# Kernel tuning notes

Measured on AMD Instinct MI355X. Metric: run time of the kernel, lower is better.

Reference implementation:

```python
import jax, jax.numpy as jnp
import numpy as np

H = 16  # num_heads

def setup_inputs() -> dict:
    key = jax.random.key(0)
    ks = jax.random.split(key, 6)
    B, T, C, S = 2, 2048, 1024, 2048
    return {
        "q": jax.random.normal(ks[0], (B, T, C), jnp.float32),
        "k_xl": jax.random.normal(ks[1], (B, S, C), jnp.float32),
        "v_xl": jax.random.normal(ks[2], (B, S, C), jnp.float32),
        "W_qkv": jax.random.normal(ks[3], (3 * C, C), jnp.float32) * (1.0 / np.sqrt(C)),
        "W_proj": jax.random.normal(ks[4], (C, C), jnp.float32) * (1.0 / np.sqrt(C)),
        "pos_emb": jax.random.normal(ks[5], (S, C), jnp.float32),
        "is_causal": 0,
    }

def reference(q, k_xl, v_xl, W_qkv, W_proj, pos_emb, is_causal):
    B, T, C = q.shape
    hd = C // H
    # self_attention: W_qkv(q).split(d_model, -1)
    qkv = jnp.einsum('btc,dc->btd', q, W_qkv)  # [B,T,3C]
    qn, kn, vn = jnp.split(qkv, 3, axis=-1)
    # XL cache gets positional embedding added before use
    kx = k_xl + pos_emb[None, :, :]            # [B,S,C]
    vx = v_xl

    def to_heads(x):
        b, s, c = x.shape
        return x.reshape(b, s, H, hd).transpose(0, 2, 1, 3)  # [B,H,s,hd]

    qh = to_heads(qn)
    kcat = jnp.concatenate([to_heads(kx), to_heads(kn)], axis=2)  # [B,H,S+T,hd]
    vcat = jnp.concatenate([to_heads(vx), to_heads(vn)], axis=2)
    scale = 1.0 / jnp.sqrt(jnp.asarray(hd, qh.dtype))
    scores = jnp.einsum('bhtd,bhsd->bhts', qh, kcat) * scale  # [B,H,T,S+T]
    attn = jax.nn.softmax(scores, axis=-1)
    y = jnp.einsum('bhts,bhsd->bhtd', attn, vcat)  # [B,H,T,hd]
    y = y.transpose(0, 2, 1, 3).reshape(B, T, C)
    return jnp.einsum('btc,dc->btd', y, W_proj)
```

## Files before the change

kernel.cpp:

```cpp
#include <hip/hip_runtime.h>

typedef unsigned short u16;
typedef unsigned int u32;
typedef u16 u16x4 __attribute__((ext_vector_type(4)));
typedef u16 u16x8 __attribute__((ext_vector_type(8)));
typedef __bf16 bf16x8 __attribute__((ext_vector_type(8)));
typedef float f32x4 __attribute__((ext_vector_type(4)));
typedef float f32x16 __attribute__((ext_vector_type(16)));

static __device__ __forceinline__ u16 f2bf(float f) {
  union { float f; u32 u; } x; x.f = f;
  u32 r = x.u + 0x7fffu + ((x.u >> 16) & 1u);
  return (u16)(r >> 16);
}
static __device__ __forceinline__ u32 packbf(float a, float b) {
  union { u32 u; __bf16 h[2]; } x; x.h[0] = (__bf16)a; x.h[1] = (__bf16)b; return x.u;
}
static __device__ __forceinline__ void pl32swap(u32& a, u32& b) {
  asm volatile("v_permlane32_swap_b32 %0, %1" : "+v"(a), "+v"(b));
}
static __device__ __forceinline__ void gload16(const void* g, void* l) {
  __builtin_amdgcn_global_load_lds((const __attribute__((address_space(1))) unsigned int*)g,
                                   (__attribute__((address_space(3))) unsigned int*)l, 16, 0, 0);
}

__global__ __launch_bounds__(256) void cvt_fuse(const float* __restrict__ q, const float* __restrict__ wqkv_f,
                                                const float* __restrict__ wproj_f, const float* __restrict__ k_xl,
                                                const float* __restrict__ pos, u16* __restrict__ qbf,
                                                u16* __restrict__ wqkv, u16* __restrict__ wproj,
                                                u16* __restrict__ khxl, float sc) {
  int i = blockIdx.x * 256 + threadIdx.x;
  if (i < 2097152) {
    const float* src;
    u16* dst;
    int j;
    float s = 1.0f;
    if (i < 1048576) { src = q; dst = qbf; j = i; }
    else if (i < 1835008) { j = i - 1048576; src = wqkv_f; dst = wqkv; if (j < 262144) s = sc; }
    else { j = i - 1835008; src = wproj_f; dst = wproj; }
    float4 v = reinterpret_cast<const float4*>(src)[j];
    u16x4 o; o[0] = f2bf(v.x * s); o[1] = f2bf(v.y * s); o[2] = f2bf(v.z * s); o[3] = f2bf(v.w * s);
    reinterpret_cast<u16x4*>(dst)[j] = o;
  } else {
    int idx = i - 2097152;
    int d8 = idx & 7;
    int s = (idx >> 3) & 2047;
    int bh = idx >> 14;
    int b = bh >> 4, h = bh & 15;
    size_t src = ((size_t)(b * 2048 + s)) * 1024 + h * 64 + d8 * 8;
    size_t ps = ((size_t)s) * 1024 + h * 64 + d8 * 8;
    float4 a0 = *(const float4*)&k_xl[src];
    float4 a1 = *(const float4*)&k_xl[src + 4];
    float4 p0 = *(const float4*)&pos[ps];
    float4 p1 = *(const float4*)&pos[ps + 4];
    u16x8 o;
    o[0] = f2bf(a0.x + p0.x); o[1] = f2bf(a0.y + p0.y); o[2] = f2bf(a0.z + p0.z); o[3] = f2bf(a0.w + p0.w);
    o[4] = f2bf(a1.x + p1.x); o[5] = f2bf(a1.y + p1.y); o[6] = f2bf(a1.z + p1.z); o[7] = f2bf(a1.w + p1.w);
    *(u16x8*)&khxl[((size_t)bh * 2048 + s) * 64 + d8 * 8] = o;
  }
}

template <int OUT_BF16>
__global__ __launch_bounds__(256, 2) void gemm_bt4(const u16* __restrict__ A, const u16* __restrict__ B,
                                                   void* __restrict__ Cout, int M, int N, int K) {
  __shared__ alignas(128) u16 As[2][8192];
  __shared__ alignas(128) u16 Bs[2][8192];
  const int tid = threadIdx.x;
  const int nbx = gridDim.x;
  const int nwg = nbx * gridDim.y;
  const int id = blockIdx.x + blockIdx.y * nbx;
  const int swz = (id & 7) * (nwg >> 3) + (id >> 3);
  const int m0 = (swz / nbx) * 128, n0 = (swz % nbx) * 128;
  const int wid = tid >> 6, lane = tid & 63;
  const int lm = lane & 15, lg = lane >> 4;
  const int wm = (wid >> 1) * 64, wn = (wid & 1) * 64;
  int srow[4], scol[4], dsto[4];
#pragma unroll
  for (int i = 0; i < 4; i++) {
    int li = tid + i * 256;
    srow[i] = li >> 3;
    scol[i] = ((li & 7) ^ (srow[i] & 7)) * 8;
    dsto[i] = (i * 256 + wid * 64) * 8;
  }
  f32x4 acc[4][4] = {};
#pragma unroll
  for (int i = 0; i < 4; i++) {
    gload16(&A[(size_t)(m0 + srow[i]) * K + scol[i]], &As[0][dsto[i]]);
    gload16(&B[(size_t)(n0 + srow[i]) * K + scol[i]], &Bs[0][dsto[i]]);
  }
  int cur = 0;
  for (int k0 = 0; k0 < K; k0 += 64) {
    __syncthreads();
    if (k0 + 64 < K) {
#pragma unroll
      for (int i = 0; i < 4; i++) {
        gload16(&A[(size_t)(m0 + srow[i]) * K + k0 + 64 + scol[i]], &As[cur ^ 1][dsto[i]]);
        gload16(&B[(size_t)(n0 + srow[i]) * K + k0 + 64 + scol[i]], &Bs[cur ^ 1][dsto[i]]);
      }
    }
    const u16* Asb = As[cur];
    const u16* Bsb = Bs[cur];
#pragma unroll
    for (int ks = 0; ks < 2; ks++) {
      bf16x8 af[4], bfr[4];
#pragma unroll
      for (int mi = 0; mi < 4; mi++) {
        int row = wm + mi * 16 + lm;
        af[mi] = *(const bf16x8*)&Asb[row * 64 + (((ks * 4 + lg) ^ (row & 7)) << 3)];
      }
#pragma unroll
      for (int ni = 0; ni < 4; ni++) {
        int row = wn + ni * 16 + lm;
        bfr[ni] = *(const bf16x8*)&Bsb[row * 64 + (((ks * 4 + lg) ^ (row & 7)) << 3)];
      }
#pragma unroll
      for (int mi = 0; mi < 4; mi++)
#pragma unroll
        for (int ni = 0; ni < 4; ni++)
          acc[mi][ni] = __builtin_amdgcn_mfma_f32_16x16x32_bf16(af[mi], bfr[ni], acc[mi][ni], 0, 0, 0);
    }
    cur ^= 1;
  }
#pragma unroll
  for (int mi = 0; mi < 4; mi++)
#pragma unroll
    for (int ni = 0; ni < 4; ni++)
#pragma unroll
      for (int r = 0; r < 4; r++) {
        int row = m0 + wm + mi * 16 + lg * 4 + r;
        int col = n0 + wn + ni * 16 + lm;
        if (OUT_BF16) ((u16*)Cout)[(size_t)row * N + col] = f2bf(acc[mi][ni][r]);
        else          ((float*)Cout)[(size_t)row * N + col] = acc[mi][ni][r];
      }
}

__global__ __launch_bounds__(256) void build_vt(const float* __restrict__ v_xl, const u16* __restrict__ qkvb,
                                                u16* __restrict__ Vt) {
  __shared__ u16 tile[64][72];
  const int bh = blockIdx.y, b = bh >> 4, h = bh & 15;
  const int s0 = blockIdx.x * 64;
  const int tid = threadIdx.x;
  {
    int sl = tid >> 2;
    int dseg = (tid & 3) * 16;
    if (s0 < 2048) {
      const float* src = v_xl + ((size_t)(b * 2048 + s0 + sl)) * 1024 + h * 64 + dseg;
#pragma unroll
      for (int j = 0; j < 16; j += 4) {
        float4 v = *(const float4*)&src[j];
        tile[sl][dseg + j] = f2bf(v.x);
        tile[sl][dseg + j + 1] = f2bf(v.y);
        tile[sl][dseg + j + 2] = f2bf(v.z);
        tile[sl][dseg + j + 3] = f2bf(v.w);
      }
    } else {
      const u16* src = qkvb + ((size_t)(b * 2048 + s0 - 2048 + sl)) * 3072 + 2048 + h * 64 + dseg;
      *(u16x8*)&tile[sl][dseg] = *(const u16x8*)&src[0];
      *(u16x8*)&tile[sl][dseg + 8] = *(const u16x8*)&src[8];
    }
  }
  __syncthreads();
  {
    int d = tid >> 2;
    int sseg = (tid & 3) * 16;
    u16* dst = Vt + ((size_t)bh * 64 + d) * 4096 + s0 + sseg;
    u16x8 o0, o1;
#pragma unroll
    for (int j = 0; j < 8; j++) { o0[j] = tile[sseg + j][d]; o1[j] = tile[sseg + 8 + j][d]; }
    *(u16x8*)&dst[0] = o0;
    *(u16x8*)&dst[8] = o1;
  }
}

__global__ __launch_bounds__(256, 2) void attn_fwd10(const u16* __restrict__ qkvb, const u16* __restrict__ khxl,
                                                     const u16* __restrict__ vt, u16* __restrict__ Y) {
  const int T = 2048;
  __shared__ alignas(128) u16 lds[16384];
  __shared__ float CBl[128];
  const int dd = blockIdx.x + (blockIdx.y << 4);
  const int w = ((dd & 7) << 6) + (dd >> 3);
  const int bh = w >> 4;
  const int q0 = (w & 15) * 128;
  const int tid = threadIdx.x, wid = tid >> 6, lane = tid & 63;
  const int qt = wid >> 1, ks = wid & 1;
  const int l31 = lane & 31, hi = lane >> 5;
  const int sw = l31 & 7;
  const int b = bh >> 4, h = bh & 15;
  bf16x8 qf0[4], qf1[4];
  {
    const u16* Qp0 = qkvb + (size_t)(b * T + q0 + qt * 64 + l31) * 3072 + h * 64;
    const u16* Qp1 = Qp0 + (size_t)32 * 3072;
#pragma unroll
    for (int c = 0; c < 4; c++) {
      qf0[c] = *(const bf16x8*)&Qp0[c * 16 + hi * 8];
      qf1[c] = *(const bf16x8*)&Qp1[c * 16 + hi * 8];
    }
  }
  const int srow = tid >> 3, pc = tid & 7;
  const int scol = (pc ^ (srow & 7)) * 8;
  const u16* kxl_s = khxl + ((size_t)bh * 2048 + srow) * 64 + scol;
  const u16* knew_s = qkvb + (size_t)(b * T + srow) * 3072 + 1024 + h * 64 + scol;
  const u16* v_s = vt + ((size_t)bh * 64 + srow) * 4096 + scol;
  const int kd = tid * 8;
  f32x16 acc00 = {0.0f}, acc01 = {0.0f}, acc10 = {0.0f}, acc11 = {0.0f};
  float lrun0 = 0.0f, lrun1 = 0.0f;
  const int krow = ks * 32 + l31;

#define STAGE_XL(KO, VO)                              \
  do {                                                \
    gload16(kxl_s, &lds[(KO) + kd]);                  \
    gload16(kxl_s + 2048, &lds[(KO) + 2048 + kd]);    \
    gload16(v_s, &lds[(VO) + kd]);                    \
    gload16(v_s + 131072, &lds[(VO) + 2048 + kd]);    \
    kxl_s += 4096; v_s += 64;                         \
  } while (0)
#define STAGE_NEW(KO, VO)                             \
  do {                                                \
    gload16(knew_s, &lds[(KO) + kd]);                 \
    gload16(knew_s + 98304, &lds[(KO) + 2048 + kd]);  \
    gload16(v_s, &lds[(VO) + kd]);                    \
    gload16(v_s + 131072, &lds[(VO) + 2048 + kd]);    \
    knew_s += 196608; v_s += 64;                      \
  } while (0)
#define COMPUTE(KO, VO)                                                             \
  do {                                                                              \
    bf16x8 kf0 = *(const bf16x8*)&lds[(KO) + krow * 64 + (((0 + hi) ^ sw) << 3)];   \
    bf16x8 kf1 = *(const bf16x8*)&lds[(KO) + krow * 64 + (((2 + hi) ^ sw) << 3)];   \
    bf16x8 kf2 = *(const bf16x8*)&lds[(KO) + krow * 64 + (((4 + hi) ^ sw) << 3)];   \
    bf16x8 kf3 = *(const bf16x8*)&lds[(KO) + krow * 64 + (((6 + hi) ^ sw) << 3)];   \
    f32x16 s0 = {0.0f}, s1 = {0.0f};                                                \
    __builtin_amdgcn_s_setprio(1);                                                  \
    s0 = __builtin_amdgcn_mfma_f32_32x32x16_bf16(kf0, qf0[0], s0, 0, 0, 0);         \
    s1 = __builtin_amdgcn_mfma_f32_32x32x16_bf16(kf0, qf1[0], s1, 0, 0, 0);         \
    s0 = __builtin_amdgcn_mfma_f32_32x32x16_bf16(kf1, qf0[1], s0, 0, 0, 0);         \
    s1 = __builtin_amdgcn_mfma_f32_32x32x16_bf16(kf1, qf1[1], s1, 0, 0, 0);         \
    s0 = __builtin_amdgcn_mfma_f32_32x32x16_bf16(kf2, qf0[2], s0, 0, 0, 0);         \
    s1 = __builtin_amdgcn_mfma_f32_32x32x16_bf16(kf2, qf1[2], s1, 0, 0, 0);         \
    s0 = __builtin_amdgcn_mfma_f32_32x32x16_bf16(kf3, qf0[3], s0, 0, 0, 0);         \
    s1 = __builtin_amdgcn_mfma_f32_32x32x16_bf16(kf3, qf1[3], s1, 0, 0, 0);         \
    __builtin_amdgcn_s_setprio(0);                                                  \
    u32 w40[4][2], w41[4][2];                                                       \
    _Pragma("unroll")                                                               \
    for (int r = 0; r < 16; r++) s0[r] = __builtin_amdgcn_exp2f(s0[r]);             \
    lrun0 += (((s0[0] + s0[1]) + (s0[2] + s0[3])) + ((s0[4] + s0[5]) + (s0[6] + s0[7])))         \
           + (((s0[8] + s0[9]) + (s0[10] + s0[11])) + ((s0[12] + s0[13]) + (s0[14] + s0[15])));  \
    _Pragma("unroll")                                                               \
    for (int g = 0; g < 4; g++) {                                                   \
      w40[g][0] = packbf(s0[4 * g + 0], s0[4 * g + 1]);                             \
      w40[g][1] = packbf(s0[4 * g + 2], s0[4 * g + 3]);                             \
    }                                                                               \
    _Pragma("unroll")                                                               \
    for (int r = 0; r < 16; r++) s1[r] = __builtin_amdgcn_exp2f(s1[r]);             \
    lrun1 += (((s1[0] + s1[1]) + (s1[2] + s1[3])) + ((s1[4] + s1[5]) + (s1[6] + s1[7])))         \
           + (((s1[8] + s1[9]) + (s1[10] + s1[11])) + ((s1[12] + s1[13]) + (s1[14] + s1[15])));  \
    _Pragma("unroll")                                                               \
    for (int g = 0; g < 4; g++) {                                                   \
      w41[g][0] = packbf(s1[4 * g + 0], s1[4 * g + 1]);                             \
      w41[g][1] = packbf(s1[4 * g + 2], s1[4 * g + 3]);                             \
    }                                                                               \
    __builtin_amdgcn_s_setprio(1);                                                  \
    _Pragma("unroll")                                                               \
    for (int m2 = 0; m2 < 2; m2++) {                                                \
      int cg = 2 * (ks * 2 + m2) + hi;                                              \
      bf16x8 v0 = *(const bf16x8*)&lds[(VO) + l31 * 64 + ((cg ^ sw) << 3)];         \
      bf16x8 v1 = *(const bf16x8*)&lds[(VO) + (32 + l31) * 64 + ((cg ^ sw) << 3)];  \
      u32 A0 = w40[2 * m2][0], A2 = w40[2 * m2 + 1][0];                             \
      pl32swap(A0, A2);                                                             \
      u32 A1 = w40[2 * m2][1], A3 = w40[2 * m2 + 1][1];                             \
      pl32swap(A1, A3);                                                             \
      union { u32 u[4]; bf16x8 v; } pf0;                                            \
      pf0.u[0] = A0; pf0.u[1] = A1; pf0.u[2] = A2; pf0.u[3] = A3;                   \
      acc00 = __builtin_amdgcn_mfma_f32_32x32x16_bf16(v0, pf0.v, acc00, 0, 0, 0);   \
      acc01 = __builtin_amdgcn_mfma_f32_32x32x16_bf16(v1, pf0.v, acc01, 0, 0, 0);   \
      u32 B0 = w41[2 * m2][0], B2 = w41[2 * m2 + 1][0];                             \
      pl32swap(B0, B2);                                                             \
      u32 B1 = w41[2 * m2][1], B3 = w41[2 * m2 + 1][1];                             \
      pl32swap(B1, B3);                                                             \
      union { u32 u[4]; bf16x8 v; } pf1;                                            \
      pf1.u[0] = B0; pf1.u[1] = B1; pf1.u[2] = B2; pf1.u[3] = B3;                   \
      acc10 = __builtin_amdgcn_mfma_f32_32x32x16_bf16(v0, pf1.v, acc10, 0, 0, 0);   \
      acc11 = __builtin_amdgcn_mfma_f32_32x32x16_bf16(v1, pf1.v, acc11, 0, 0, 0);   \
    }                                                                               \
    __builtin_amdgcn_s_setprio(0);                                                  \
  } while (0)

  STAGE_XL(0, 8192);
  for (int j = 0; j < 15; ++j) {
    __syncthreads();
    STAGE_XL(4096, 12288);
    COMPUTE(0, 8192);
    __syncthreads();
    STAGE_XL(0, 8192);
    COMPUTE(4096, 12288);
  }
  __syncthreads();
  STAGE_XL(4096, 12288);
  COMPUTE(0, 8192);
  __syncthreads();
  STAGE_NEW(0, 8192);
  COMPUTE(4096, 12288);
  for (int j = 0; j < 15; ++j) {
    __syncthreads();
    STAGE_NEW(4096, 12288);
    COMPUTE(0, 8192);
    __syncthreads();
    STAGE_NEW(0, 8192);
    COMPUTE(4096, 12288);
  }
  __syncthreads();
  STAGE_NEW(4096, 12288);
  COMPUTE(0, 8192);
  __syncthreads();
  COMPUTE(4096, 12288);
#undef STAGE_XL
#undef STAGE_NEW
#undef COMPUTE

  float lt0 = lrun0 + __shfl_xor(lrun0, 32);
  float lt1 = lrun1 + __shfl_xor(lrun1, 32);
  __syncthreads();
  float* CB = (float*)lds;
  if (ks) {
    float* p0 = CB + (size_t)(qt * 2 + 0) * 64 * 32 + (size_t)lane * 32;
    float* p1 = CB + (size_t)(qt * 2 + 1) * 64 * 32 + (size_t)lane * 32;
#pragma unroll
    for (int j = 0; j < 8; j++) {
      f32x4 u0, u1;
#pragma unroll
      for (int e = 0; e < 4; e++) {
        u0[e] = (j < 4) ? acc00[4 * j + e] : acc01[4 * (j - 4) + e];
        u1[e] = (j < 4) ? acc10[4 * j + e] : acc11[4 * (j - 4) + e];
      }
      *(f32x4*)&p0[4 * (j ^ (lane & 7))] = u0;
      *(f32x4*)&p1[4 * (j ^ (lane & 7))] = u1;
    }
    if (hi == 0) {
      CBl[(qt * 2 + 0) * 32 + l31] = lt0;
      CBl[(qt * 2 + 1) * 32 + l31] = lt1;
    }
  }
  __syncthreads();
  if (!ks) {
    const float* p0 = CB + (size_t)(qt * 2 + 0) * 64 * 32 + (size_t)lane * 32;
    const float* p1 = CB + (size_t)(qt * 2 + 1) * 64 * 32 + (size_t)lane * 32;
#pragma unroll
    for (int j = 0; j < 8; j++) {
      f32x4 u0 = *(const f32x4*)&p0[4 * (j ^ (lane & 7))];
      f32x4 u1 = *(const f32x4*)&p1[4 * (j ^ (lane & 7))];
#pragma unroll
      for (int e = 0; e < 4; e++) {
        if (j < 4) { acc00[4 * j + e] += u0[e]; acc10[4 * j + e] += u1[e]; }
        else       { acc01[4 * (j - 4) + e] += u0[e]; acc11[4 * (j - 4) + e] += u1[e]; }
      }
    }
    lt0 += CBl[(qt * 2 + 0) * 32 + l31];
    lt1 += CBl[(qt * 2 + 1) * 32 + l31];
    float inv0 = 1.0f / lt0;
    float inv1 = 1.0f / lt1;
#pragma unroll
    for (int qb = 0; qb < 2; qb++) {
      float inv = qb ? inv1 : inv0;
      u16* Ts = (u16*)((char*)lds + (qt * 2 + qb) * 8192);
#pragma unroll
      for (int dt = 0; dt < 2; dt++)
#pragma unroll
        for (int r2 = 0; r2 < 4; r2++) {
          u16x4 o;
#pragma unroll
          for (int e = 0; e < 4; e++) {
            float v;
            if (qb == 0) v = dt ? acc01[4 * r2 + e] : acc00[4 * r2 + e];
            else         v = dt ? acc11[4 * r2 + e] : acc10[4 * r2 + e];
            o[e] = f2bf(v * inv);
          }
          int dbase = dt * 32 + r2 * 8 + hi * 4;
          int byteoff = l31 * 128 + ((dbase * 2) ^ (sw << 4));
          *(u16x4*)((char*)Ts + byteoff) = o;
        }
#pragma unroll
      for (int p4 = 0; p4 < 4; p4++) {
        int row = p4 * 8 + (lane >> 3);
        int c16 = lane & 7;
        u16x8 v = *(const u16x8*)((const char*)Ts + row * 128 + ((c16 << 4) ^ ((row & 7) << 4)));
        *(u16x8*)&Y[((size_t)(b * T + q0 + qt * 64 + qb * 32 + row)) * 1024 + h * 64 + c16 * 8] = v;
      }
    }
  }
}

extern "C" void kernel_launch(void* const* d_in, const int* in_sizes, int n_in,
                              void* d_out, int out_size, void* d_ws, size_t ws_size,
                              hipStream_t stream) {
  const float* q = (const float*)d_in[0];
  const float* k_xl = (const float*)d_in[1];
  const float* v_xl = (const float*)d_in[2];
  const float* W_qkv = (const float*)d_in[3];
  const float* W_proj = (const float*)d_in[4];
  const float* pos = (const float*)d_in[5];

  u16* wqkv = (u16*)d_ws;
  u16* wproj = wqkv + (size_t)3072 * 1024;
  u16* qbf = wproj + (size_t)1024 * 1024;
  u16* qkvb = qbf + (size_t)4096 * 1024;
  u16* khxl = qkvb + (size_t)4096 * 3072;
  u16* vt = khxl + (size_t)4 * 1024 * 1024;
  u16* ybf = vt + (size_t)8 * 1024 * 1024;

  const float SC = 0.125f * 1.4426950408889634f;

  cvt_fuse<<<10240, 256, 0, stream>>>(q, W_qkv, W_proj, k_xl, pos, qbf, wqkv, wproj, khxl, SC);

  gemm_bt4<1><<<dim3(24, 32), 256, 0, stream>>>(qbf, wqkv, qkvb, 4096, 3072, 1024);

  build_vt<<<dim3(64, 32), 256, 0, stream>>>(v_xl, qkvb, vt);

  attn_fwd10<<<dim3(16, 32), 256, 0, stream>>>(qkvb, khxl, vt, ybf);

  gemm_bt4<0><<<dim3(8, 32), 256, 0, stream>>>(ybf, wproj, d_out, 4096, 1024, 1024);
}
```

Before: 164.2 us.

## Split attention over XL and new key halves with separate combine kernel

Adds an attention kernel that gives each query tile two blocks, one for the XL-cache half of the keys and one for the new-token half. Each block writes unnormalised fp32 partial outputs and row sums to workspace, and a small combine kernel adds the two halves, normalises and writes bf16. The aim is more parallelism and shorter per-block serial loops. The cost is an extra launch plus fp32 partial traffic to and from global memory. This path runs only when the workspace is large enough; otherwise the original fused kernel is used.

```diff
diff --git a/kernel.cpp b/kernel.cpp
--- a/kernel.cpp
+++ b/kernel.cpp
@@ -172,57 +172,7 @@
   }
 }
 
-__global__ __launch_bounds__(256, 2) void attn_fwd10(const u16* __restrict__ qkvb, const u16* __restrict__ khxl,
-                                                     const u16* __restrict__ vt, u16* __restrict__ Y) {
-  const int T = 2048;
-  __shared__ alignas(128) u16 lds[16384];
-  __shared__ float CBl[128];
-  const int dd = blockIdx.x + (blockIdx.y << 4);
-  const int w = ((dd & 7) << 6) + (dd >> 3);
-  const int bh = w >> 4;
-  const int q0 = (w & 15) * 128;
-  const int tid = threadIdx.x, wid = tid >> 6, lane = tid & 63;
-  const int qt = wid >> 1, ks = wid & 1;
-  const int l31 = lane & 31, hi = lane >> 5;
-  const int sw = l31 & 7;
-  const int b = bh >> 4, h = bh & 15;
-  bf16x8 qf0[4], qf1[4];
-  {
-    const u16* Qp0 = qkvb + (size_t)(b * T + q0 + qt * 64 + l31) * 3072 + h * 64;
-    const u16* Qp1 = Qp0 + (size_t)32 * 3072;
-#pragma unroll
-    for (int c = 0; c < 4; c++) {
-      qf0[c] = *(const bf16x8*)&Qp0[c * 16 + hi * 8];
-      qf1[c] = *(const bf16x8*)&Qp1[c * 16 + hi * 8];
-    }
-  }
-  const int srow = tid >> 3, pc = tid & 7;
-  const int scol = (pc ^ (srow & 7)) * 8;
-  const u16* kxl_s = khxl + ((size_t)bh * 2048 + srow) * 64 + scol;
-  const u16* knew_s = qkvb + (size_t)(b * T + srow) * 3072 + 1024 + h * 64 + scol;
-  const u16* v_s = vt + ((size_t)bh * 64 + srow) * 4096 + scol;
-  const int kd = tid * 8;
-  f32x16 acc00 = {0.0f}, acc01 = {0.0f}, acc10 = {0.0f}, acc11 = {0.0f};
-  float lrun0 = 0.0f, lrun1 = 0.0f;
-  const int krow = ks * 32 + l31;
-
-#define STAGE_XL(KO, VO)                              \
-  do {                                                \
-    gload16(kxl_s, &lds[(KO) + kd]);                  \
-    gload16(kxl_s + 2048, &lds[(KO) + 2048 + kd]);    \
-    gload16(v_s, &lds[(VO) + kd]);                    \
-    gload16(v_s + 131072, &lds[(VO) + 2048 + kd]);    \
-    kxl_s += 4096; v_s += 64;                         \
-  } while (0)
-#define STAGE_NEW(KO, VO)                             \
-  do {                                                \
-    gload16(knew_s, &lds[(KO) + kd]);                 \
-    gload16(knew_s + 98304, &lds[(KO) + 2048 + kd]);  \
-    gload16(v_s, &lds[(VO) + kd]);                    \
-    gload16(v_s + 131072, &lds[(VO) + 2048 + kd]);    \
-    knew_s += 196608; v_s += 64;                      \
-  } while (0)
-#define COMPUTE(KO, VO)                                                             \
+#define ATTN_COMPUTE(KO, VO)                                                        \
   do {                                                                              \
     bf16x8 kf0 = *(const bf16x8*)&lds[(KO) + krow * 64 + (((0 + hi) ^ sw) << 3)];   \
     bf16x8 kf1 = *(const bf16x8*)&lds[(KO) + krow * 64 + (((2 + hi) ^ sw) << 3)];   \
@@ -284,37 +234,224 @@
     __builtin_amdgcn_s_setprio(0);                                                  \
   } while (0)
 
+__global__ __launch_bounds__(256, 2) void attn_split(const u16* __restrict__ qkvb, const u16* __restrict__ khxl,
+                                                     const u16* __restrict__ vt, float* __restrict__ gpart,
+                                                     float* __restrict__ gl) {
+  const int T = 2048;
+  __shared__ alignas(128) u16 lds[16384];
+  __shared__ float CBl[128];
+  const int z = blockIdx.z;
+  const int dd = blockIdx.x + (blockIdx.y << 4);
+  const int w = ((dd & 7) << 6) + (dd >> 3);
+  const int bh = w >> 4;
+  const int q0 = (w & 15) * 128;
+  const int tid = threadIdx.x, wid = tid >> 6, lane = tid & 63;
+  const int qt = wid >> 1, ks = wid & 1;
+  const int l31 = lane & 31, hi = lane >> 5;
+  const int sw = l31 & 7;
+  const int b = bh >> 4, h = bh & 15;
+  bf16x8 qf0[4], qf1[4];
+  {
+    const u16* Qp0 = qkvb + (size_t)(b * T + q0 + qt * 64 + l31) * 3072 + h * 64;
+    const u16* Qp1 = Qp0 + (size_t)32 * 3072;
+#pragma unroll
+    for (int c = 0; c < 4; c++) {
+      qf0[c] = *(const bf16x8*)&Qp0[c * 16 + hi * 8];
+      qf1[c] = *(const bf16x8*)&Qp1[c * 16 + hi * 8];
+    }
+  }
+  const int srow = tid >> 3, pc = tid & 7;
+  const int scol = (pc ^ (srow & 7)) * 8;
+  const u16* kp = z ? (qkvb + (size_t)(b * T + srow) * 3072 + 1024 + h * 64 + scol)
+                    : (khxl + ((size_t)bh * 2048 + srow) * 64 + scol);
+  const size_t kstep = z ? (size_t)196608 : (size_t)4096;
+  const size_t kc2  = z ? (size_t)98304 : (size_t)2048;
+  const u16* v_s = vt + ((size_t)bh * 64 + srow) * 4096 + z * 2048 + scol;
+  const int kd = tid * 8;
+  f32x16 acc00 = {0.0f}, acc01 = {0.0f}, acc10 = {0.0f}, acc11 = {0.0f};
+  float lrun0 = 0.0f, lrun1 = 0.0f;
+  const int krow = ks * 32 + l31;
+
+#define STAGE_Z(KO, VO)                               \
+  do {                                                \
+    gload16(kp, &lds[(KO) + kd]);                     \
+    gload16(kp + kc2, &lds[(KO) + 2048 + kd]);        \
+    gload16(v_s, &lds[(VO) + kd]);                    \
+    gload16(v_s + 131072, &lds[(VO) + 2048 + kd]);    \
+    kp += kstep; v_s += 64;                           \
+  } while (0)
+
+  STAGE_Z(0, 8192);
+  for (int j = 0; j < 15; ++j) {
+    __syncthreads();
+    STAGE_Z(4096, 12288);
+    ATTN_COMPUTE(0, 8192);
+    __syncthreads();
+    STAGE_Z(0, 8192);
+    ATTN_COMPUTE(4096, 12288);
+  }
+  __syncthreads();
+  STAGE_Z(4096, 12288);
+  ATTN_COMPUTE(0, 8192);
+  __syncthreads();
+  ATTN_COMPUTE(4096, 12288);
+#undef STAGE_Z
+
+  float lt0 = lrun0 + __shfl_xor(lrun0, 32);
+  float lt1 = lrun1 + __shfl_xor(lrun1, 32);
+  __syncthreads();
+  float* CB = (float*)lds;
+  if (ks) {
+    float* p0 = CB + (size_t)(qt * 2 + 0) * 64 * 32 + (size_t)lane * 32;
+    float* p1 = CB + (size_t)(qt * 2 + 1) * 64 * 32 + (size_t)lane * 32;
+#pragma unroll
+    for (int j = 0; j < 8; j++) {
+      f32x4 u0, u1;
+#pragma unroll
+      for (int e = 0; e < 4; e++) {
+        u0[e] = (j < 4) ? acc00[4 * j + e] : acc01[4 * (j - 4) + e];
+        u1[e] = (j < 4) ? acc10[4 * j + e] : acc11[4 * (j - 4) + e];
+      }
+      *(f32x4*)&p0[4 * (j ^ (lane & 7))] = u0;
+      *(f32x4*)&p1[4 * (j ^ (lane & 7))] = u1;
+    }
+    if (hi == 0) {
+      CBl[(qt * 2 + 0) * 32 + l31] = lt0;
+      CBl[(qt * 2 + 1) * 32 + l31] = lt1;
+    }
+  }
+  __syncthreads();
+  if (!ks) {
+    const float* p0 = CB + (size_t)(qt * 2 + 0) * 64 * 32 + (size_t)lane * 32;
+    const float* p1 = CB + (size_t)(qt * 2 + 1) * 64 * 32 + (size_t)lane * 32;
+#pragma unroll
+    for (int j = 0; j < 8; j++) {
+      f32x4 u0 = *(const f32x4*)&p0[4 * (j ^ (lane & 7))];
+      f32x4 u1 = *(const f32x4*)&p1[4 * (j ^ (lane & 7))];
+#pragma unroll
+      for (int e = 0; e < 4; e++) {
+        if (j < 4) { acc00[4 * j + e] += u0[e]; acc10[4 * j + e] += u1[e]; }
+        else       { acc01[4 * (j - 4) + e] += u0[e]; acc11[4 * (j - 4) + e] += u1[e]; }
+      }
+    }
+    lt0 += CBl[(qt * 2 + 0) * 32 + l31];
+    lt1 += CBl[(qt * 2 + 1) * 32 + l31];
+    float* gp = gpart + (size_t)z * (32u * 2048 * 64) + ((size_t)bh * 2048 + q0 + qt * 64) * 64;
+#pragma unroll
+    for (int r = 0; r < 16; r++) {
+      int d = (r & 3) + 8 * (r >> 2) + 4 * hi;
+      gp[(size_t)l31 * 64 + d]             = acc00[r];
+      gp[(size_t)l31 * 64 + 32 + d]        = acc01[r];
+      gp[(size_t)(32 + l31) * 64 + d]      = acc10[r];
+      gp[(size_t)(32 + l31) * 64 + 32 + d] = acc11[r];
+    }
+    if (hi == 0) {
+      float* glp = gl + (size_t)z * (32u * 2048) + (size_t)bh * 2048 + q0 + qt * 64;
+      glp[l31] = lt0;
+      glp[32 + l31] = lt1;
+    }
+  }
+}
+
+__global__ __launch_bounds__(256) void attn_comb(const float* __restrict__ gpart, const float* __restrict__ gl,
+                                                 u16* __restrict__ ybf) {
+  int idx = blockIdx.x * 256 + threadIdx.x;
+  int d4 = idx & 15;
+  int q = (idx >> 4) & 2047;
+  int bh = idx >> 15;
+  int b = bh >> 4, h = bh & 15;
+  size_t qi = (size_t)bh * 2048 + q;
+  const size_t zoff = (size_t)32 * 2048 * 64;
+  f32x4 a0 = *(const f32x4*)&gpart[qi * 64 + d4 * 4];
+  f32x4 a1 = *(const f32x4*)&gpart[zoff + qi * 64 + d4 * 4];
+  float inv = 1.0f / (gl[qi] + gl[(size_t)32 * 2048 + qi]);
+  u16x4 o;
+#pragma unroll
+  for (int e = 0; e < 4; e++) o[e] = f2bf((a0[e] + a1[e]) * inv);
+  *(u16x4*)&ybf[(size_t)(b * 2048 + q) * 1024 + h * 64 + d4 * 4] = o;
+}
+
+__global__ __launch_bounds__(256, 2) void attn_fwd10(const u16* __restrict__ qkvb, const u16* __restrict__ khxl,
+                                                     const u16* __restrict__ vt, u16* __restrict__ Y) {
+  const int T = 2048;
+  __shared__ alignas(128) u16 lds[16384];
+  __shared__ float CBl[128];
+  const int dd = blockIdx.x + (blockIdx.y << 4);
+  const int w = ((dd & 7) << 6) + (dd >> 3);
+  const int bh = w >> 4;
+  const int q0 = (w & 15) * 128;
+  const int tid = threadIdx.x, wid = tid >> 6, lane = tid & 63;
+  const int qt = wid >> 1, ks = wid & 1;
+  const int l31 = lane & 31, hi = lane >> 5;
+  const int sw = l31 & 7;
+  const int b = bh >> 4, h = bh & 15;
+  bf16x8 qf0[4], qf1[4];
+  {
+    const u16* Qp0 = qkvb + (size_t)(b * T + q0 + qt * 64 + l31) * 3072 + h * 64;
+    const u16* Qp1 = Qp0 + (size_t)32 * 3072;
+#pragma unroll
+    for (int c = 0; c < 4; c++) {
+      qf0[c] = *(const bf16x8*)&Qp0[c * 16 + hi * 8];
+      qf1[c] = *(const bf16x8*)&Qp1[c * 16 + hi * 8];
+    }
+  }
+  const int srow = tid >> 3, pc = tid & 7;
+  const int scol = (pc ^ (srow & 7)) * 8;
+  const u16* kxl_s = khxl + ((size_t)bh * 2048 + srow) * 64 + scol;
+  const u16* knew_s = qkvb + (size_t)(b * T + srow) * 3072 + 1024 + h * 64 + scol;
+  const u16* v_s = vt + ((size_t)bh * 64 + srow) * 4096 + scol;
+  const int kd = tid * 8;
+  f32x16 acc00 = {0.0f}, acc01 = {0.0f}, acc10 = {0.0f}, acc11 = {0.0f};
+  float lrun0 = 0.0f, lrun1 = 0.0f;
+  const int krow = ks * 32 + l31;
+
+#define STAGE_XL(KO, VO)                              \
+  do {                                                \
+    gload16(kxl_s, &lds[(KO) + kd]);                  \
+    gload16(kxl_s + 2048, &lds[(KO) + 2048 + kd]);    \
+    gload16(v_s, &lds[(VO) + kd]);                    \
+    gload16(v_s + 131072, &lds[(VO) + 2048 + kd]);    \
+    kxl_s += 4096; v_s += 64;                         \
+  } while (0)
+#define STAGE_NEW(KO, VO)                             \
+  do {                                                \
+    gload16(knew_s, &lds[(KO) + kd]);                 \
+    gload16(knew_s + 98304, &lds[(KO) + 2048 + kd]);  \
+    gload16(v_s, &lds[(VO) + kd]);                    \
+    gload16(v_s + 131072, &lds[(VO) + 2048 + kd]);    \
+    knew_s += 196608; v_s += 64;                      \
+  } while (0)
+
   STAGE_XL(0, 8192);
   for (int j = 0; j < 15; ++j) {
     __syncthreads();
     STAGE_XL(4096, 12288);
-    COMPUTE(0, 8192);
+    ATTN_COMPUTE(0, 8192);
     __syncthreads();
     STAGE_XL(0, 8192);
-    COMPUTE(4096, 12288);
+    ATTN_COMPUTE(4096, 12288);
   }
   __syncthreads();
   STAGE_XL(4096, 12288);
-  COMPUTE(0, 8192);
+  ATTN_COMPUTE(0, 8192);
   __syncthreads();
   STAGE_NEW(0, 8192);
-  COMPUTE(4096, 12288);
+  ATTN_COMPUTE(4096, 12288);
   for (int j = 0; j < 15; ++j) {
     __syncthreads();
     STAGE_NEW(4096, 12288);
-    COMPUTE(0, 8192);
+    ATTN_COMPUTE(0, 8192);
     __syncthreads();
     STAGE_NEW(0, 8192);
-    COMPUTE(4096, 12288);
+    ATTN_COMPUTE(4096, 12288);
   }
   __syncthreads();
   STAGE_NEW(4096, 12288);
-  COMPUTE(0, 8192);
-  __syncthreads();
-  COMPUTE(4096, 12288);
+  ATTN_COMPUTE(0, 8192);
+  __syncthreads();
+  ATTN_COMPUTE(4096, 12288);
 #undef STAGE_XL
 #undef STAGE_NEW
-#undef COMPUTE
 
   float lt0 = lrun0 + __shfl_xor(lrun0, 32);
   float lt1 = lrun1 + __shfl_xor(lrun1, 32);
@@ -405,6 +542,9 @@
   u16* khxl = qkvb + (size_t)4096 * 3072;
   u16* vt = khxl + (size_t)4 * 1024 * 1024;
   u16* ybf = vt + (size_t)8 * 1024 * 1024;
+  float* gpart = (float*)(ybf + (size_t)4 * 1024 * 1024);
+  float* gl = gpart + (size_t)2 * 32 * 2048 * 64;
+  size_t need = (size_t)((char*)(gl + (size_t)2 * 32 * 2048) - (char*)d_ws);
 
   const float SC = 0.125f * 1.4426950408889634f;
 
@@ -414,7 +554,12 @@
 
   build_vt<<<dim3(64, 32), 256, 0, stream>>>(v_xl, qkvb, vt);
 
-  attn_fwd10<<<dim3(16, 32), 256, 0, stream>>>(qkvb, khxl, vt, ybf);
+  if (ws_size >= need) {
+    attn_split<<<dim3(16, 32, 2), 256, 0, stream>>>(qkvb, khxl, vt, gpart, gl);
+    attn_comb<<<4096, 256, 0, stream>>>(gpart, gl, ybf);
+  } else {
+    attn_fwd10<<<dim3(16, 32), 256, 0, stream>>>(qkvb, khxl, vt, ybf);
+  }
 
   gemm_bt4<0><<<dim3(8, 32), 256, 0, stream>>>(ybf, wproj, d_out, 4096, 1024, 1024);
 }
```

Result: slower. 178.2 us (+8.5%).
